# Kernel tuning notes

Hardware: AMD Instinct MI355X
Metric: run time of the kernel (lower is better)

The kernel has to match this reference:

```python
import jax, jax.numpy as jnp
import numpy as np

INPUT_SIZE = 1024
OUTPUT_SIZE = 1024
B, S = 4, 2048


def setup_inputs() -> dict:
    key = jax.random.key(0)
    k1, k2, k3, k4, k5, k6 = jax.random.split(key, 6)
    scale = 1.0 / np.sqrt(INPUT_SIZE)
    return {
        "inputs_for_keys": jax.random.normal(k1, (B, S, INPUT_SIZE), jnp.float32),
        "inputs_for_values": jax.random.normal(k2, (B, S, INPUT_SIZE), jnp.float32),
        "inputs_for_queries": jax.random.normal(k3, (B, S, INPUT_SIZE), jnp.float32),
        "W_k": jax.random.normal(k4, (INPUT_SIZE, OUTPUT_SIZE), jnp.float32) * scale,
        "W_v": jax.random.normal(k5, (INPUT_SIZE, OUTPUT_SIZE), jnp.float32) * scale,
        "W_q": jax.random.normal(k6, (INPUT_SIZE, OUTPUT_SIZE), jnp.float32) * scale,
    }


def reference(inputs_for_keys, inputs_for_values, inputs_for_queries, W_k, W_v, W_q):
    # Linear projections (bias=False): x @ W  -> [B, S, D_out]
    K = jnp.einsum("bsi,io->bso", inputs_for_keys, W_k)
    V = jnp.einsum("bsi,io->bso", inputs_for_values, W_v)
    Q = jnp.einsum("bqi,io->bqo", inputs_for_queries, W_q)
    d_k = K.shape[-1]
    # scores: [B, Sq, Sk], scaled by sqrt(embedding_size of K)
    scores = jnp.einsum("bqd,bkd->bqk", Q, K) / jnp.sqrt(jnp.asarray(d_k, Q.dtype))
    # causal mask: positions k > q masked to -inf (use_mask=True since is_self_attention)
    q_idx = jnp.arange(Q.shape[1])[:, None]
    k_idx = jnp.arange(K.shape[1])[None, :]
    scores = jnp.where(k_idx > q_idx, jnp.asarray(-jnp.inf, scores.dtype), scores)
    weights = jax.nn.softmax(scores, axis=-1)
    # output: [B, Sq, D_out]
    return jnp.einsum("bqk,bkd->bqd", weights, V)
```

## Files before the change

kernel.cpp:

```cpp
#include <hip/hip_runtime.h>


typedef __attribute__((ext_vector_type(8))) short short8;
typedef __attribute__((ext_vector_type(4))) float floatx4;

static constexpr long long XE = 8388608LL;
static constexpr long long WE = 1048576LL;

static __device__ __forceinline__ unsigned short f2b(float f) {
  unsigned u = __builtin_bit_cast(unsigned, f);
  u = (u + 0x7fffu + ((u >> 16) & 1u)) >> 16;
  return (unsigned short)u;
}

static __device__ __forceinline__ void gload16(const unsigned short* g, unsigned short* l) {
  __builtin_amdgcn_global_load_lds(
      (const __attribute__((address_space(1))) unsigned int*)g,
      (__attribute__((address_space(3))) unsigned int*)l, 16, 0, 0);
}

#define VMCNT(n) asm volatile("s_waitcnt vmcnt(" #n ")" ::: "memory")
#define LGKM0() asm volatile("s_waitcnt lgkmcnt(0)" ::: "memory")
#define BARRIER() do { asm volatile("" ::: "memory"); __builtin_amdgcn_s_barrier(); asm volatile("" ::: "memory"); } while (0)

#define STAGE(base, matoff, h, slot, kt) do {                                  \
    const unsigned short* _s = (base) + (h) * 131072 + (kt) * 64;              \
    char* _d = sb + (slot) * 65536 + (matoff) + (h) * 16384 + dwave;           \
    gload16(_s, (unsigned short*)_d);                                          \
    gload16(_s + 65536, (unsigned short*)(_d + 8192));                         \
  } while (0)

#define READ_A(slot, mb) do {                                                  \
    const char* _p = sb + (slot) * 65536 + aoffb + (mb) * 2048;                \
    af[0][0] = *(const short8*)(_p + c0);        af[0][1] = *(const short8*)(_p + c1); \
    af[1][0] = *(const short8*)(_p + 2048 + c0); af[1][1] = *(const short8*)(_p + 2048 + c1); \
    af[2][0] = *(const short8*)(_p + 4096 + c0); af[2][1] = *(const short8*)(_p + 4096 + c1); \
    af[3][0] = *(const short8*)(_p + 6144 + c0); af[3][1] = *(const short8*)(_p + 6144 + c1); \
  } while (0)

#define READ_B(slot, nb, bfx) do {                                             \
    const char* _p = sb + (slot) * 65536 + boffb + (nb) * 2048;                \
    bfx[0][0] = *(const short8*)(_p + c0);        bfx[0][1] = *(const short8*)(_p + c1); \
    bfx[1][0] = *(const short8*)(_p + 2048 + c0); bfx[1][1] = *(const short8*)(_p + 2048 + c1); \
  } while (0)

#define MF16(MB, NB, bfx) do {                                                 \
    __builtin_amdgcn_s_setprio(1);                                             \
    _Pragma("unroll")                                                          \
    for (int _m = 0; _m < 4; ++_m) {                                           \
      _Pragma("unroll")                                                        \
      for (int _n = 0; _n < 2; ++_n) {                                         \
        acc[(MB) + _m][(NB) + _n] = __builtin_amdgcn_mfma_f32_16x16x32_bf16(   \
            af[_m][0], bfx[_n][0], acc[(MB) + _m][(NB) + _n], 0, 0, 0);        \
        acc[(MB) + _m][(NB) + _n] = __builtin_amdgcn_mfma_f32_16x16x32_bf16(   \
            af[_m][1], bfx[_n][1], acc[(MB) + _m][(NB) + _n], 0, 0, 0);        \
      } }                                                                      \
    __builtin_amdgcn_s_setprio(0);                                             \
  } while (0)

__global__ __launch_bounds__(512, 2) void projTV8(
    const unsigned short* __restrict__ Xb, const unsigned short* __restrict__ WvT,
    const unsigned short* __restrict__ Gt, unsigned short* __restrict__ Tb,
    unsigned short* __restrict__ Vt) {
  extern __shared__ char sb[];
  const int orig = blockIdx.x;
  const int w = (orig & 7) * 32 + (orig >> 3);
  const unsigned short *Aop, *Bop;
  unsigned short* C;
  int ldc, bi, bj;
  if (w < 128) { Aop = Xb + XE; Bop = Gt; C = Tb; ldc = 1024; bi = w >> 2; bj = w & 3; }
  else { const int j = w - 128; Aop = WvT; Bop = Xb; C = Vt; ldc = 8192; bi = j & 3; bj = j >> 2; }

  const int tid = threadIdx.x, wave = tid >> 6, lane = tid & 63;
  const int wm = wave >> 2, wn = wave & 3, frow = lane & 15, hi = lane >> 4;
  const int r0 = tid >> 3, p0 = ((tid & 7) ^ (r0 & 7)) * 8;
  const int dwave = wave * 1024;
  const int sx = frow & 7;
  const int c0 = (hi ^ sx) * 16, c1 = ((4 + hi) ^ sx) * 16;
  const int aoffb = (wm * 128 + frow) * 128;
  const int boffb = 32768 + (wn * 64 + frow) * 128;
  const unsigned short* Ab = Aop + (long long)(bi * 256 + r0) * 1024 + p0;
  const unsigned short* Bb = Bop + (long long)(bj * 256 + r0) * 1024 + p0;

  short8 af[4][2], bf0[2][2], bf1[2][2];
  floatx4 acc[8][4] = {};

  STAGE(Ab, 0, 0, 0, 0);     STAGE(Ab, 0, 1, 0, 0);
  STAGE(Bb, 32768, 0, 0, 0); STAGE(Bb, 32768, 1, 0, 0);
  STAGE(Bb, 32768, 0, 1, 1); STAGE(Bb, 32768, 1, 1, 1);
  VMCNT(4);
  BARRIER();

  for (int t = 0; t < 8; ++t) {
    const int kt1 = 2 * t + 1, kt2 = 2 * t + 2, kt3 = 2 * t + 3;
    const bool pf = t < 7;
    READ_A(0, 0); READ_B(0, 0, bf0);
    STAGE(Ab, 0, 0, 1, kt1);
    BARRIER(); LGKM0();
    MF16(0, 0, bf0);
    BARRIER();
    READ_B(0, 2, bf1);
    STAGE(Ab, 0, 1, 1, kt1);
    BARRIER(); LGKM0();
    MF16(0, 2, bf1);
    BARRIER();
    READ_A(0, 4);
    if (pf) STAGE(Bb, 32768, 0, 0, kt2);
    BARRIER(); LGKM0();
    MF16(4, 2, bf1);
    BARRIER();
    if (pf) STAGE(Bb, 32768, 1, 0, kt2);
    BARRIER();
    MF16(4, 0, bf0);
    if (pf) { VMCNT(4); } else { VMCNT(0); }
    BARRIER();
    READ_A(1, 0); READ_B(1, 0, bf0);
    if (pf) STAGE(Ab, 0, 0, 0, kt2);
    BARRIER(); LGKM0();
    MF16(0, 0, bf0);
    BARRIER();
    READ_B(1, 2, bf1);
    if (pf) STAGE(Ab, 0, 1, 0, kt2);
    BARRIER(); LGKM0();
    MF16(0, 2, bf1);
    BARRIER();
    READ_A(1, 4);
    if (pf) STAGE(Bb, 32768, 0, 1, kt3);
    BARRIER(); LGKM0();
    MF16(4, 2, bf1);
    BARRIER();
    if (pf) STAGE(Bb, 32768, 1, 1, kt3);
    BARRIER();
    MF16(4, 0, bf0);
    if (pf) { VMCNT(4); } else { VMCNT(0); }
    BARRIER();
  }

  const long long crow0 = (long long)bi * 256 + wm * 128 + hi * 4;
  const int ccol = bj * 256 + wn * 64 + frow;
#pragma unroll
  for (int m = 0; m < 8; ++m)
#pragma unroll
    for (int j = 0; j < 4; ++j) {
      unsigned short* cp = C + (crow0 + m * 16 + j) * (long long)ldc + ccol;
#pragma unroll
      for (int n = 0; n < 4; ++n) cp[n * 16] = f2b(acc[m][n][j]);
    }
}

template <int NF>
static __device__ __forceinline__ void gemm_loop(
    const unsigned short* __restrict__ A, const unsigned short* __restrict__ Bt,
    int lda, int ldb, int nk, int bi, int bj,
    unsigned short* lA, unsigned short* lB, floatx4 acc[4][NF]) {
  const int t = threadIdx.x, wave = t >> 6, lane = t & 63;
  const int wr = wave >> 1, wc = wave & 1;
  const int sr = lane >> 3;
  const int sc = ((lane & 7) ^ sr) * 8;
  const unsigned short* gA = A + (long long)(bi * 128 + wave * 32 + sr) * lda + sc;
  const unsigned short* gB = Bt + (long long)(bj * (NF * 32) + wave * (NF * 8) + sr) * ldb + sc;
  unsigned short* lAw = lA + wave * 2048;
  unsigned short* lBw = lB + wave * (NF * 512);
  const int frow = lane & 15, hi = lane >> 4;

  for (int ks = 0; ks < nk; ++ks) {
    const long long k0 = (long long)ks * 64;
    __syncthreads();
#pragma unroll
    for (int g = 0; g < 4; ++g)
      gload16(gA + (long long)g * 8 * lda + k0, lAw + g * 512);
#pragma unroll
    for (int g = 0; g < NF; ++g)
      gload16(gB + (long long)g * 8 * ldb + k0, lBw + g * 512);
    __syncthreads();
#pragma unroll
    for (int kk = 0; kk < 2; ++kk) {
      const int ch = (kk * 4 + hi) ^ (frow & 7);
      short8 af[4], bf[NF];
#pragma unroll
      for (int m = 0; m < 4; ++m)
        af[m] = *(const short8*)&lA[(wr * 64 + m * 16 + frow) * 64 + ch * 8];
#pragma unroll
      for (int n = 0; n < NF; ++n)
        bf[n] = *(const short8*)&lB[(wc * (NF * 16) + n * 16 + frow) * 64 + ch * 8];
#pragma unroll
      for (int m = 0; m < 4; ++m)
#pragma unroll
        for (int n = 0; n < NF; ++n)
          acc[m][n] = __builtin_amdgcn_mfma_f32_16x16x32_bf16(af[m], bf[n], acc[m][n], 0, 0, 0);
    }
  }
}

__global__ __launch_bounds__(256) void gt_kernel(
    const unsigned short* __restrict__ WkB, const unsigned short* __restrict__ WqB,
    unsigned short* __restrict__ Gt) {
  __shared__ __align__(16) unsigned short lA[8192], lB[8192];
  floatx4 acc[4][4] = {};
  gemm_loop<4>(WkB, WqB, 1024, 1024, 16, blockIdx.x, blockIdx.y, lA, lB, acc);
  const int tid = threadIdx.x, wave = tid >> 6, lane = tid & 63;
  const int wr = wave >> 1, wc = wave & 1, frow = lane & 15, hi = lane >> 4;
  const long long crow0 = (long long)blockIdx.x * 128 + wr * 64 + hi * 4;
  const int ccol = blockIdx.y * 128 + wc * 64 + frow;
#pragma unroll
  for (int m = 0; m < 4; ++m)
#pragma unroll
    for (int j = 0; j < 4; ++j) {
      unsigned short* cp = Gt + (crow0 + m * 16 + j) * 1024 + ccol;
#pragma unroll
      for (int n = 0; n < 4; ++n) cp[n * 16] = f2b(acc[m][n][j]);
    }
}

__global__ __launch_bounds__(256) void scores_exp(
    const unsigned short* __restrict__ Tb, const unsigned short* __restrict__ Xk,
    unsigned short* __restrict__ P, float* __restrict__ Rpart) {
  __shared__ __align__(16) unsigned short lA[8192], lB[4096];
  const int orig = blockIdx.x;
  const int w = (orig & 7) * 136 + (orig >> 3);
  const int b = w / 272;
  int t2 = w - b * 272;
  int bi = 0;
  while (t2 >= 2 * bi + 2) { t2 -= 2 * bi + 2; ++bi; }
  const int bj = t2;

  floatx4 acc[4][2] = {};
  gemm_loop<2>(Tb + (long long)b * 2048 * 1024, Xk + (long long)b * 2048 * 1024,
               1024, 1024, 16, bi, bj, lA, lB, acc);

  const int tid = threadIdx.x, wave = tid >> 6, lane = tid & 63;
  const int wr = wave >> 1, wc = wave & 1, frow = lane & 15, hi = lane >> 4;
  const bool diag = (bj >= 2 * bi);
  float rp[4][4];
#pragma unroll
  for (int m = 0; m < 4; ++m)
#pragma unroll
    for (int j = 0; j < 4; ++j) {
      const int rloc = wr * 64 + hi * 4 + m * 16 + j;
      const int rglob = bi * 128 + rloc;
      float s = 0.f;
#pragma unroll
      for (int n = 0; n < 2; ++n) {
        const int cglob = bj * 64 + wc * 32 + n * 16 + frow;
        float e = __expf(acc[m][n][j] * 0.03125f);
        if (diag && cglob > rglob) e = 0.f;
        acc[m][n][j] = e;
        s += e;
      }
      rp[m][j] = s;
    }
#pragma unroll
  for (int m = 0; m < 4; ++m)
#pragma unroll
    for (int j = 0; j < 4; ++j) {
      rp[m][j] += __shfl_xor(rp[m][j], 1);
      rp[m][j] += __shfl_xor(rp[m][j], 2);
      rp[m][j] += __shfl_xor(rp[m][j], 4);
      rp[m][j] += __shfl_xor(rp[m][j], 8);
    }
  unsigned short* C = P + (long long)b * 2048 * 2048;
  const long long crow0 = (long long)bi * 128 + wr * 64 + hi * 4;
  const int ccol = bj * 64 + wc * 32 + frow;
#pragma unroll
  for (int m = 0; m < 4; ++m)
#pragma unroll
    for (int j = 0; j < 4; ++j) {
      unsigned short* cp = C + (crow0 + m * 16 + j) * 2048LL + ccol;
      cp[0] = f2b(acc[m][0][j]);
      cp[16] = f2b(acc[m][1][j]);
    }
  __syncthreads();
  float* red = (float*)lA;
  if (frow == 0) {
#pragma unroll
    for (int m = 0; m < 4; ++m)
#pragma unroll
      for (int j = 0; j < 4; ++j)
        red[(wr * 64 + hi * 4 + m * 16 + j) * 2 + wc] = rp[m][j];
  }
  __syncthreads();
  if (tid < 128)
    Rpart[((long long)b * 32 + bj) * 2048 + bi * 128 + tid] = red[tid * 2] + red[tid * 2 + 1];
}

__global__ __launch_bounds__(256) void rowsum(
    const float* __restrict__ Rpart, float* __restrict__ Rinv) {
  const int t = blockIdx.x * 256 + threadIdx.x;
  const int b = t >> 11, row = t & 2047;
  const int nb = (row >> 6) + 1;
  float s = 0.f;
  for (int bj = 0; bj < nb; ++bj) s += Rpart[(b * 32 + bj) * 2048 + row];
  Rinv[t] = 1.f / s;
}

__global__ __launch_bounds__(256) void pv_kernel(
    const unsigned short* __restrict__ P, const unsigned short* __restrict__ Vt,
    const float* __restrict__ Rinv, float* __restrict__ out) {
  __shared__ __align__(16) unsigned short lA[8192], lB[4096];
  const int orig = blockIdx.x;
  const int c = orig & 7, i = orig >> 3;
  const int bi = 15 - (i >> 3);
  const int rr = (i & 7) + c * 8;
  const int b = rr >> 4, bj = rr & 15;
  floatx4 acc[4][2] = {};
  gemm_loop<2>(P + (long long)b * 2048 * 2048, Vt + (long long)b * 2048, 2048, 8192,
               (bi + 1) * 2, bi, bj, lA, lB, acc);
  const int tid = threadIdx.x, wave = tid >> 6, lane = tid & 63;
  const int wr = wave >> 1, wc = wave & 1, frow = lane & 15, hi = lane >> 4;
  float* C = out + (long long)b * 2048 * 1024;
  const float* Ri = Rinv + b * 2048;
#pragma unroll
  for (int m = 0; m < 4; ++m)
#pragma unroll
    for (int j = 0; j < 4; ++j) {
      const int row = bi * 128 + wr * 64 + hi * 4 + m * 16 + j;
      const float riv = Ri[row];
      float* cp = C + (long long)row * 1024 + bj * 64 + wc * 32 + frow;
      cp[0] = acc[m][0][j] * riv;
      cp[16] = acc[m][1][j] * riv;
    }
}

__global__ __launch_bounds__(256) void cvtX(
    const float* __restrict__ Xk, const float* __restrict__ Xv,
    const float* __restrict__ Xq, unsigned short* __restrict__ Xb) {
  const int bx = blockIdx.x, t = threadIdx.x;
  const int y = bx >> 10, sub = bx & 1023;
  const float* in = y == 0 ? Xv : (y == 1 ? Xq : Xk);
  unsigned short* o = Xb + (long long)y * XE;
  const int n8 = (int)(XE / 8), stride = 1024 * 256;
  for (int i = sub * 256 + t; i < n8; i += stride) {
    const floatx4* src = (const floatx4*)in + 2 * (long long)i;
    floatx4 a = __builtin_nontemporal_load(src);
    floatx4 d = __builtin_nontemporal_load(src + 1);
    short8 v;
    v[0] = (short)f2b(a[0]); v[1] = (short)f2b(a[1]);
    v[2] = (short)f2b(a[2]); v[3] = (short)f2b(a[3]);
    v[4] = (short)f2b(d[0]); v[5] = (short)f2b(d[1]);
    v[6] = (short)f2b(d[2]); v[7] = (short)f2b(d[3]);
    __builtin_nontemporal_store(v, (short8*)o + i);
  }
}

__global__ __launch_bounds__(256) void cvtW(
    const float* __restrict__ Wq, const float* __restrict__ Wk,
    const float* __restrict__ Wv, unsigned short* __restrict__ WqB,
    unsigned short* __restrict__ WkB, unsigned short* __restrict__ WvT) {
  __shared__ unsigned short tile[64][65];
  const int bx = blockIdx.x, t = threadIdx.x;
  if (bx < 128) {
    const int y = bx >> 6, sub = bx & 63;
    const float* in = y == 0 ? Wq : Wk;
    unsigned short* o = y == 0 ? WqB : WkB;
    const int n8 = (int)(WE / 8), stride = 64 * 256;
    for (int i = sub * 256 + t; i < n8; i += stride) {
      const float4* src = (const float4*)in + 2 * (long long)i;
      float4 a = src[0], d = src[1];
      short8 v;
      v[0] = (short)f2b(a.x); v[1] = (short)f2b(a.y);
      v[2] = (short)f2b(a.z); v[3] = (short)f2b(a.w);
      v[4] = (short)f2b(d.x); v[5] = (short)f2b(d.y);
      v[6] = (short)f2b(d.z); v[7] = (short)f2b(d.w);
      ((short8*)o)[i] = v;
    }
  } else {
    const int v = bx - 128;
    const int i0 = (v & 15) * 64, j0 = (v >> 4) * 64;
#pragma unroll
    for (int r = 0; r < 16; ++r) {
      int lin = r * 256 + t;
      int i = lin >> 6, j = lin & 63;
      tile[i][j] = f2b(Wv[(long long)(i0 + i) * 1024 + j0 + j]);
    }
    __syncthreads();
#pragma unroll
    for (int r = 0; r < 16; ++r) {
      int lin = r * 256 + t;
      int o = lin >> 6, i = lin & 63;
      WvT[(long long)(j0 + o) * 1024 + i0 + i] = tile[i][o];
    }
  }
}

extern "C" void kernel_launch(void* const* d_in, const int* in_sizes, int n_in,
                              void* d_out, int out_size, void* d_ws, size_t ws_size,
                              hipStream_t stream) {
  const float* Xk = (const float*)d_in[0];
  const float* Xv = (const float*)d_in[1];
  const float* Xq = (const float*)d_in[2];
  const float* Wk = (const float*)d_in[3];
  const float* Wv = (const float*)d_in[4];
  const float* Wq = (const float*)d_in[5];
  float* out = (float*)d_out;

  unsigned short* ws = (unsigned short*)d_ws;
  unsigned short* Xb = ws;
  unsigned short* WqB = ws + 3 * XE;
  unsigned short* WkB = WqB + WE;
  unsigned short* WvT = WkB + WE;
  unsigned short* Gt = WvT + WE;
  unsigned short* Tb = Gt + WE;
  unsigned short* Vt = Tb + XE;
  float* Rpart = (float*)(Vt + XE);
  float* Rinv = Rpart + 4 * 32 * 2048;
  unsigned short* Pbuf = ws;

  cvtW<<<384, 256, 0, stream>>>(Wq, Wk, Wv, WqB, WkB, WvT);
  gt_kernel<<<dim3(8, 8), 256, 0, stream>>>(WkB, WqB, Gt);
  cvtX<<<3072, 256, 0, stream>>>(Xk, Xv, Xq, Xb);
  projTV8<<<256, 512, 131072, stream>>>(Xb, WvT, Gt, Tb, Vt);
  scores_exp<<<1088, 256, 0, stream>>>(Tb, Xb + 2 * XE, Pbuf, Rpart);
  rowsum<<<32, 256, 0, stream>>>(Rpart, Rinv);
  pv_kernel<<<1024, 256, 0, stream>>>(Pbuf, Vt, Rinv, out);
}
```

Measured before the change: 173.3 us.

## Fuse fp32-to-bf16 input conversion into projection and scores GEMM loads

Removes the separate cvtX kernel. The projection and score GEMMs now read fp32 activations directly, convert them to bf16 in registers and write them to LDS, while the bf16 operand still goes through direct global-to-LDS loads. The scores kernel is replaced with a 256x256-tile, 512-thread version using the same shared mainloop, so there are 144 triangular tiles and rowsum reads 8 partials instead of 32. The gain is avoiding a full write and re-read of the bf16 activations. The cost is twice the global read bytes per operand inside the GEMMs, more register pressure (launch bounds go from 2 to 1 blocks per CU), and coarser causal tiles that waste more masked work on the diagonal and give fewer blocks.

```diff
diff --git a/kernel.cpp b/kernel.cpp
--- a/kernel.cpp
+++ b/kernel.cpp
@@ -23,12 +23,6 @@
 #define LGKM0() asm volatile("s_waitcnt lgkmcnt(0)" ::: "memory")
 #define BARRIER() do { asm volatile("" ::: "memory"); __builtin_amdgcn_s_barrier(); asm volatile("" ::: "memory"); } while (0)
 
-#define STAGE(base, matoff, h, slot, kt) do {                                  \
-    const unsigned short* _s = (base) + (h) * 131072 + (kt) * 64;              \
-    char* _d = sb + (slot) * 65536 + (matoff) + (h) * 16384 + dwave;           \
-    gload16(_s, (unsigned short*)_d);                                          \
-    gload16(_s + 65536, (unsigned short*)(_d + 8192));                         \
-  } while (0)
 
 #define READ_A(slot, mb) do {                                                  \
     const char* _p = sb + (slot) * 65536 + aoffb + (mb) * 2048;                \
@@ -58,19 +52,126 @@
     __builtin_amdgcn_s_setprio(0);                                             \
   } while (0)
 
-__global__ __launch_bounds__(512, 2) void projTV8(
-    const unsigned short* __restrict__ Xb, const unsigned short* __restrict__ WvT,
-    const unsigned short* __restrict__ Gt, unsigned short* __restrict__ Tb,
-    unsigned short* __restrict__ Vt) {
+#define FLOAD(st, h, kt) do {                                                  \
+    const float* _s = F + (h) * 131072 + (kt) * 64;                            \
+    fr[st][0] = *(const floatx4*)_s;                                           \
+    fr[st][1] = *(const floatx4*)(_s + 4);                                     \
+    fr[st][2] = *(const floatx4*)(_s + 65536);                                 \
+    fr[st][3] = *(const floatx4*)(_s + 65540);                                 \
+  } while (0)
+
+#define FWRITE(st, h, slot) do {                                               \
+    char* _d = sb + (slot) * 65536 + FOFF + (h) * 16384 + dwave + lane * 16;   \
+    short8 _v0, _v1;                                                           \
+    _Pragma("unroll")                                                          \
+    for (int _e = 0; _e < 4; ++_e) {                                           \
+      _v0[_e]     = (short)f2b(fr[st][0][_e]);                                 \
+      _v0[_e + 4] = (short)f2b(fr[st][1][_e]);                                 \
+      _v1[_e]     = (short)f2b(fr[st][2][_e]);                                 \
+      _v1[_e + 4] = (short)f2b(fr[st][3][_e]);                                 \
+    }                                                                          \
+    *(short8*)_d = _v0;                                                        \
+    *(short8*)(_d + 8192) = _v1;                                               \
+  } while (0)
+
+#define GSTAGE(h, slot, kt) do {                                               \
+    const unsigned short* _s = G + (h) * 131072 + (kt) * 64;                   \
+    char* _d = sb + (slot) * 65536 + GOFF + (h) * 16384 + dwave;               \
+    gload16(_s, (unsigned short*)_d);                                          \
+    gload16(_s + 65536, (unsigned short*)(_d + 8192));                         \
+  } while (0)
+
+template <int BF32>
+static __device__ __forceinline__ void kloop8m(
+    const float* F, const unsigned short* G, char* sb,
+    int dwave, int lane, int aoffb, int boffb, int c0, int c1,
+    floatx4 (&acc)[8][4]) {
+  short8 af[4][2], bf0[2][2], bf1[2][2];
+  constexpr int FOFF = BF32 ? 32768 : 0;
+  constexpr int GOFF = BF32 ? 0 : 32768;
+  floatx4 fr[4][4];
+
+  if constexpr (!BF32) {
+    FLOAD(0, 0, 0); FLOAD(1, 1, 0);
+    GSTAGE(0, 0, 0); GSTAGE(1, 0, 0);
+    GSTAGE(0, 1, 1); GSTAGE(1, 1, 1);
+    FWRITE(0, 0, 0); FWRITE(1, 1, 0);
+    VMCNT(4);
+  } else {
+    GSTAGE(0, 0, 0); GSTAGE(1, 0, 0);
+    FLOAD(0, 0, 0); FLOAD(1, 1, 0);
+    FLOAD(2, 0, 1); FLOAD(3, 1, 1);
+    FWRITE(0, 0, 0); FWRITE(1, 1, 0);
+  }
+  LGKM0();
+  BARRIER();
+
+  for (int t = 0; t < 8; ++t) {
+    const int kt1 = 2 * t + 1, kt2 = 2 * t + 2, kt3 = 2 * t + 3;
+    const bool pf = t < 7;
+    READ_A(0, 0); READ_B(0, 0, bf0);
+    if constexpr (!BF32) { FLOAD(0, 0, kt1); } else { GSTAGE(0, 1, kt1); }
+    BARRIER(); LGKM0();
+    MF16(0, 0, bf0);
+    BARRIER();
+    READ_B(0, 2, bf1);
+    if constexpr (!BF32) { FLOAD(1, 1, kt1); } else { GSTAGE(1, 1, kt1); }
+    BARRIER(); LGKM0();
+    MF16(0, 2, bf1);
+    BARRIER();
+    READ_A(0, 4);
+    if (pf) { if constexpr (!BF32) { GSTAGE(0, 0, kt2); } else { FLOAD(0, 0, kt2); } }
+    BARRIER(); LGKM0();
+    MF16(4, 2, bf1);
+    BARRIER();
+    if (pf) { if constexpr (!BF32) { GSTAGE(1, 0, kt2); } else { FLOAD(1, 1, kt2); } }
+    BARRIER();
+    MF16(4, 0, bf0);
+    if constexpr (!BF32) {
+      FWRITE(0, 0, 1); FWRITE(1, 1, 1);
+      if (pf) { VMCNT(4); } else { VMCNT(0); }
+    } else {
+      FWRITE(2, 0, 1); FWRITE(3, 1, 1);
+      if (pf) { VMCNT(8); } else { VMCNT(0); }
+    }
+    LGKM0();
+    BARRIER();
+    READ_A(1, 0); READ_B(1, 0, bf0);
+    if (pf) { if constexpr (!BF32) { FLOAD(2, 0, kt2); } else { GSTAGE(0, 0, kt2); } }
+    BARRIER(); LGKM0();
+    MF16(0, 0, bf0);
+    BARRIER();
+    READ_B(1, 2, bf1);
+    if (pf) { if constexpr (!BF32) { FLOAD(3, 1, kt2); } else { GSTAGE(1, 0, kt2); } }
+    BARRIER(); LGKM0();
+    MF16(0, 2, bf1);
+    BARRIER();
+    READ_A(1, 4);
+    if (pf) { if constexpr (!BF32) { GSTAGE(0, 1, kt3); } else { FLOAD(2, 0, kt3); } }
+    BARRIER(); LGKM0();
+    MF16(4, 2, bf1);
+    BARRIER();
+    if (pf) { if constexpr (!BF32) { GSTAGE(1, 1, kt3); } else { FLOAD(3, 1, kt3); } }
+    BARRIER();
+    MF16(4, 0, bf0);
+    if (pf) {
+      if constexpr (!BF32) { FWRITE(2, 0, 0); FWRITE(3, 1, 0); VMCNT(4); }
+      else                 { FWRITE(0, 0, 0); FWRITE(1, 1, 0); VMCNT(8); }
+      LGKM0();
+    } else {
+      VMCNT(0);
+    }
+    BARRIER();
+  }
+}
+
+__global__ __launch_bounds__(512, 1) void projTV8(
+    const float* __restrict__ Xq, const float* __restrict__ Xv,
+    const unsigned short* __restrict__ WvT, const unsigned short* __restrict__ Gt,
+    unsigned short* __restrict__ Tb, unsigned short* __restrict__ Vt) {
   extern __shared__ char sb[];
   const int orig = blockIdx.x;
   const int w = (orig & 7) * 32 + (orig >> 3);
-  const unsigned short *Aop, *Bop;
-  unsigned short* C;
-  int ldc, bi, bj;
-  if (w < 128) { Aop = Xb + XE; Bop = Gt; C = Tb; ldc = 1024; bi = w >> 2; bj = w & 3; }
-  else { const int j = w - 128; Aop = WvT; Bop = Xb; C = Vt; ldc = 8192; bi = j & 3; bj = j >> 2; }
-
   const int tid = threadIdx.x, wave = tid >> 6, lane = tid & 63;
   const int wm = wave >> 2, wn = wave & 3, frow = lane & 15, hi = lane >> 4;
   const int r0 = tid >> 3, p0 = ((tid & 7) ^ (r0 & 7)) * 8;
@@ -79,61 +180,21 @@
   const int c0 = (hi ^ sx) * 16, c1 = ((4 + hi) ^ sx) * 16;
   const int aoffb = (wm * 128 + frow) * 128;
   const int boffb = 32768 + (wn * 64 + frow) * 128;
-  const unsigned short* Ab = Aop + (long long)(bi * 256 + r0) * 1024 + p0;
-  const unsigned short* Bb = Bop + (long long)(bj * 256 + r0) * 1024 + p0;
-
-  short8 af[4][2], bf0[2][2], bf1[2][2];
+
   floatx4 acc[8][4] = {};
-
-  STAGE(Ab, 0, 0, 0, 0);     STAGE(Ab, 0, 1, 0, 0);
-  STAGE(Bb, 32768, 0, 0, 0); STAGE(Bb, 32768, 1, 0, 0);
-  STAGE(Bb, 32768, 0, 1, 1); STAGE(Bb, 32768, 1, 1, 1);
-  VMCNT(4);
-  BARRIER();
-
-  for (int t = 0; t < 8; ++t) {
-    const int kt1 = 2 * t + 1, kt2 = 2 * t + 2, kt3 = 2 * t + 3;
-    const bool pf = t < 7;
-    READ_A(0, 0); READ_B(0, 0, bf0);
-    STAGE(Ab, 0, 0, 1, kt1);
-    BARRIER(); LGKM0();
-    MF16(0, 0, bf0);
-    BARRIER();
-    READ_B(0, 2, bf1);
-    STAGE(Ab, 0, 1, 1, kt1);
-    BARRIER(); LGKM0();
-    MF16(0, 2, bf1);
-    BARRIER();
-    READ_A(0, 4);
-    if (pf) STAGE(Bb, 32768, 0, 0, kt2);
-    BARRIER(); LGKM0();
-    MF16(4, 2, bf1);
-    BARRIER();
-    if (pf) STAGE(Bb, 32768, 1, 0, kt2);
-    BARRIER();
-    MF16(4, 0, bf0);
-    if (pf) { VMCNT(4); } else { VMCNT(0); }
-    BARRIER();
-    READ_A(1, 0); READ_B(1, 0, bf0);
-    if (pf) STAGE(Ab, 0, 0, 0, kt2);
-    BARRIER(); LGKM0();
-    MF16(0, 0, bf0);
-    BARRIER();
-    READ_B(1, 2, bf1);
-    if (pf) STAGE(Ab, 0, 1, 0, kt2);
-    BARRIER(); LGKM0();
-    MF16(0, 2, bf1);
-    BARRIER();
-    READ_A(1, 4);
-    if (pf) STAGE(Bb, 32768, 0, 1, kt3);
-    BARRIER(); LGKM0();
-    MF16(4, 2, bf1);
-    BARRIER();
-    if (pf) STAGE(Bb, 32768, 1, 1, kt3);
-    BARRIER();
-    MF16(4, 0, bf0);
-    if (pf) { VMCNT(4); } else { VMCNT(0); }
-    BARRIER();
+  unsigned short* C;
+  int ldc, bi, bj;
+  if (w < 128) {
+    bi = w >> 2; bj = w & 3; C = Tb; ldc = 1024;
+    const float* F = Xq + (long long)(bi * 256 + r0) * 1024 + p0;
+    const unsigned short* G = Gt + (long long)(bj * 256 + r0) * 1024 + p0;
+    kloop8m<0>(F, G, sb, dwave, lane, aoffb, boffb, c0, c1, acc);
+  } else {
+    const int j = w - 128;
+    bi = j & 3; bj = j >> 2; C = Vt; ldc = 8192;
+    const unsigned short* G = WvT + (long long)(bi * 256 + r0) * 1024 + p0;
+    const float* F = Xv + (long long)(bj * 256 + r0) * 1024 + p0;
+    kloop8m<1>(F, G, sb, dwave, lane, aoffb, boffb, c0, c1, acc);
   }
 
   const long long crow0 = (long long)bi * 256 + wm * 128 + hi * 4;
@@ -146,6 +207,73 @@
 #pragma unroll
       for (int n = 0; n < 4; ++n) cp[n * 16] = f2b(acc[m][n][j]);
     }
+}
+
+__global__ __launch_bounds__(512, 1) void scores_exp8(
+    const unsigned short* __restrict__ Tb, const float* __restrict__ Xk,
+    unsigned short* __restrict__ P, float* __restrict__ Rpart) {
+  extern __shared__ char sb[];
+  const int orig = blockIdx.x;
+  const int w = (orig & 7) * 18 + (orig >> 3);
+  const int b = w / 36;
+  int t2 = w - b * 36;
+  int bi = 0;
+  while (t2 >= bi + 1) { t2 -= bi + 1; ++bi; }
+  const int bj = t2;
+
+  const int tid = threadIdx.x, wave = tid >> 6, lane = tid & 63;
+  const int wm = wave >> 2, wn = wave & 3, frow = lane & 15, hi = lane >> 4;
+  const int r0 = tid >> 3, p0 = ((tid & 7) ^ (r0 & 7)) * 8;
+  const int dwave = wave * 1024;
+  const int sx = frow & 7;
+  const int c0 = (hi ^ sx) * 16, c1 = ((4 + hi) ^ sx) * 16;
+  const int aoffb = (wm * 128 + frow) * 128;
+  const int boffb = 32768 + (wn * 64 + frow) * 128;
+
+  const unsigned short* G = Tb + (long long)b * 2048 * 1024 + (long long)(bi * 256 + r0) * 1024 + p0;
+  const float* F = Xk + (long long)b * 2048 * 1024 + (long long)(bj * 256 + r0) * 1024 + p0;
+
+  floatx4 acc[8][4] = {};
+  kloop8m<1>(F, G, sb, dwave, lane, aoffb, boffb, c0, c1, acc);
+
+  const bool diag = (bi == bj);
+  unsigned short* C = P + (long long)b * 2048 * 2048;
+  float rs[8][4];
+#pragma unroll
+  for (int m = 0; m < 8; ++m)
+#pragma unroll
+    for (int j = 0; j < 4; ++j) {
+      const int row_loc = wm * 128 + hi * 4 + m * 16 + j;
+      const int row_glob = bi * 256 + row_loc;
+      unsigned short* cp = C + (long long)row_glob * 2048 + bj * 256 + wn * 64 + frow;
+      float s = 0.f;
+#pragma unroll
+      for (int n = 0; n < 4; ++n) {
+        const int col = bj * 256 + wn * 64 + n * 16 + frow;
+        float e = __expf(acc[m][n][j] * 0.03125f);
+        if (diag && col > row_glob) e = 0.f;
+        cp[n * 16] = f2b(e);
+        s += e;
+      }
+      s += __shfl_xor(s, 1);
+      s += __shfl_xor(s, 2);
+      s += __shfl_xor(s, 4);
+      s += __shfl_xor(s, 8);
+      rs[m][j] = s;
+    }
+  __syncthreads();
+  float* red = (float*)sb;
+  if (frow == 0) {
+#pragma unroll
+    for (int m = 0; m < 8; ++m)
+#pragma unroll
+      for (int j = 0; j < 4; ++j)
+        red[(wm * 128 + hi * 4 + m * 16 + j) * 4 + wn] = rs[m][j];
+  }
+  __syncthreads();
+  if (tid < 256)
+    Rpart[((long long)b * 8 + bj) * 2048 + bi * 256 + tid] =
+        red[tid * 4] + red[tid * 4 + 1] + red[tid * 4 + 2] + red[tid * 4 + 3];
 }
 
 template <int NF>
@@ -212,84 +340,13 @@
     }
 }
 
-__global__ __launch_bounds__(256) void scores_exp(
-    const unsigned short* __restrict__ Tb, const unsigned short* __restrict__ Xk,
-    unsigned short* __restrict__ P, float* __restrict__ Rpart) {
-  __shared__ __align__(16) unsigned short lA[8192], lB[4096];
-  const int orig = blockIdx.x;
-  const int w = (orig & 7) * 136 + (orig >> 3);
-  const int b = w / 272;
-  int t2 = w - b * 272;
-  int bi = 0;
-  while (t2 >= 2 * bi + 2) { t2 -= 2 * bi + 2; ++bi; }
-  const int bj = t2;
-
-  floatx4 acc[4][2] = {};
-  gemm_loop<2>(Tb + (long long)b * 2048 * 1024, Xk + (long long)b * 2048 * 1024,
-               1024, 1024, 16, bi, bj, lA, lB, acc);
-
-  const int tid = threadIdx.x, wave = tid >> 6, lane = tid & 63;
-  const int wr = wave >> 1, wc = wave & 1, frow = lane & 15, hi = lane >> 4;
-  const bool diag = (bj >= 2 * bi);
-  float rp[4][4];
-#pragma unroll
-  for (int m = 0; m < 4; ++m)
-#pragma unroll
-    for (int j = 0; j < 4; ++j) {
-      const int rloc = wr * 64 + hi * 4 + m * 16 + j;
-      const int rglob = bi * 128 + rloc;
-      float s = 0.f;
-#pragma unroll
-      for (int n = 0; n < 2; ++n) {
-        const int cglob = bj * 64 + wc * 32 + n * 16 + frow;
-        float e = __expf(acc[m][n][j] * 0.03125f);
-        if (diag && cglob > rglob) e = 0.f;
-        acc[m][n][j] = e;
-        s += e;
-      }
-      rp[m][j] = s;
-    }
-#pragma unroll
-  for (int m = 0; m < 4; ++m)
-#pragma unroll
-    for (int j = 0; j < 4; ++j) {
-      rp[m][j] += __shfl_xor(rp[m][j], 1);
-      rp[m][j] += __shfl_xor(rp[m][j], 2);
-      rp[m][j] += __shfl_xor(rp[m][j], 4);
-      rp[m][j] += __shfl_xor(rp[m][j], 8);
-    }
-  unsigned short* C = P + (long long)b * 2048 * 2048;
-  const long long crow0 = (long long)bi * 128 + wr * 64 + hi * 4;
-  const int ccol = bj * 64 + wc * 32 + frow;
-#pragma unroll
-  for (int m = 0; m < 4; ++m)
-#pragma unroll
-    for (int j = 0; j < 4; ++j) {
-      unsigned short* cp = C + (crow0 + m * 16 + j) * 2048LL + ccol;
-      cp[0] = f2b(acc[m][0][j]);
-      cp[16] = f2b(acc[m][1][j]);
-    }
-  __syncthreads();
-  float* red = (float*)lA;
-  if (frow == 0) {
-#pragma unroll
-    for (int m = 0; m < 4; ++m)
-#pragma unroll
-      for (int j = 0; j < 4; ++j)
-        red[(wr * 64 + hi * 4 + m * 16 + j) * 2 + wc] = rp[m][j];
-  }
-  __syncthreads();
-  if (tid < 128)
-    Rpart[((long long)b * 32 + bj) * 2048 + bi * 128 + tid] = red[tid * 2] + red[tid * 2 + 1];
-}
-
 __global__ __launch_bounds__(256) void rowsum(
     const float* __restrict__ Rpart, float* __restrict__ Rinv) {
   const int t = blockIdx.x * 256 + threadIdx.x;
   const int b = t >> 11, row = t & 2047;
-  const int nb = (row >> 6) + 1;
+  const int nb = (row >> 8) + 1;
   float s = 0.f;
-  for (int bj = 0; bj < nb; ++bj) s += Rpart[(b * 32 + bj) * 2048 + row];
+  for (int bj = 0; bj < nb; ++bj) s += Rpart[(b * 8 + bj) * 2048 + row];
   Rinv[t] = 1.f / s;
 }
 
@@ -319,27 +376,6 @@
       cp[0] = acc[m][0][j] * riv;
       cp[16] = acc[m][1][j] * riv;
     }
-}
-
-__global__ __launch_bounds__(256) void cvtX(
-    const float* __restrict__ Xk, const float* __restrict__ Xv,
-    const float* __restrict__ Xq, unsigned short* __restrict__ Xb) {
-  const int bx = blockIdx.x, t = threadIdx.x;
-  const int y = bx >> 10, sub = bx & 1023;
-  const float* in = y == 0 ? Xv : (y == 1 ? Xq : Xk);
-  unsigned short* o = Xb + (long long)y * XE;
-  const int n8 = (int)(XE / 8), stride = 1024 * 256;
-  for (int i = sub * 256 + t; i < n8; i += stride) {
-    const floatx4* src = (const floatx4*)in + 2 * (long long)i;
-    floatx4 a = __builtin_nontemporal_load(src);
-    floatx4 d = __builtin_nontemporal_load(src + 1);
-    short8 v;
-    v[0] = (short)f2b(a[0]); v[1] = (short)f2b(a[1]);
-    v[2] = (short)f2b(a[2]); v[3] = (short)f2b(a[3]);
-    v[4] = (short)f2b(d[0]); v[5] = (short)f2b(d[1]);
-    v[6] = (short)f2b(d[2]); v[7] = (short)f2b(d[3]);
-    __builtin_nontemporal_store(v, (short8*)o + i);
-  }
 }
 
 __global__ __launch_bounds__(256) void cvtW(
@@ -394,22 +430,20 @@
   float* out = (float*)d_out;
 
   unsigned short* ws = (unsigned short*)d_ws;
-  unsigned short* Xb = ws;
-  unsigned short* WqB = ws + 3 * XE;
+  unsigned short* WqB = ws;
   unsigned short* WkB = WqB + WE;
   unsigned short* WvT = WkB + WE;
   unsigned short* Gt = WvT + WE;
   unsigned short* Tb = Gt + WE;
   unsigned short* Vt = Tb + XE;
   float* Rpart = (float*)(Vt + XE);
-  float* Rinv = Rpart + 4 * 32 * 2048;
-  unsigned short* Pbuf = ws;
+  float* Rinv = Rpart + 4 * 8 * 2048;
+  unsigned short* Pbuf = (unsigned short*)(Rinv + 8192);
 
   cvtW<<<384, 256, 0, stream>>>(Wq, Wk, Wv, WqB, WkB, WvT);
   gt_kernel<<<dim3(8, 8), 256, 0, stream>>>(WkB, WqB, Gt);
-  cvtX<<<3072, 256, 0, stream>>>(Xk, Xv, Xq, Xb);
-  projTV8<<<256, 512, 131072, stream>>>(Xb, WvT, Gt, Tb, Vt);
-  scores_exp<<<1088, 256, 0, stream>>>(Tb, Xb + 2 * XE, Pbuf, Rpart);
+  projTV8<<<256, 512, 131072, stream>>>(Xq, Xv, WvT, Gt, Tb, Vt);
+  scores_exp8<<<144, 512, 131072, stream>>>(Tb, Xk, Pbuf, Rpart);
   rowsum<<<32, 256, 0, stream>>>(Rpart, Rinv);
   pv_kernel<<<1024, 256, 0, stream>>>(Pbuf, Vt, Rinv, out);
 }
```

Measured after the change: 252.7 us. 45.8% more time.
